# Performance work log

Measured on AMD Instinct MI355X. Metric: run time of the kernel, lower is better.

Reference implementation:

```python
import jax, jax.numpy as jnp
import numpy as np

JITTER = 1e-05
TOL = 1e-04
MAX_ITER = 10
TAYLOR_ORDER = 5


def _safe_eigh(A):
    # torch safe_eigh: first attempt always adds jitter*I (eigh on SPD never fails, so first try succeeds)
    D = A.shape[-1]
    return jnp.linalg.eigh(A + JITTER * jnp.eye(D, dtype=A.dtype))


def _rebuild(vecs, vals):
    # vecs @ diag(vals) @ vecs^T, batched
    return jnp.einsum('...ij,...j,...kj->...ik', vecs, vals, vecs)


def matrix_sqrt(A):
    vals, vecs = _safe_eigh(A)
    return _rebuild(vecs, jnp.sqrt(jnp.clip(vals, JITTER)))


def matrix_inv_sqrt(A):
    vals, vecs = _safe_eigh(A)
    return _rebuild(vecs, 1.0 / jnp.sqrt(jnp.clip(vals, JITTER)))


def enforce_spd(M):
    vals, vecs = _safe_eigh(M)
    M2 = _rebuild(vecs, jnp.clip(vals, JITTER))
    return (M2 + jnp.swapaxes(M2, -1, -2)) * 0.5


def expm_taylor(Xm):
    D = Xm.shape[-1]
    I = jnp.broadcast_to(jnp.eye(D, dtype=Xm.dtype), Xm.shape)
    out = I
    Xp = I
    fac = 1.0
    for i in range(1, TAYLOR_ORDER + 1):
        Xp = Xp @ Xm
        fac *= i
        out = out + Xp / fac
    return out


def karcher_mean(X):
    # X: (B, N, D, D) SPD matrices -> (B, D, D) Riemannian (Karcher) mean
    B, N, D, _ = X.shape
    G0 = X.mean(axis=1)

    def step(carry, _):
        G, done = carry
        G_sqrt = matrix_sqrt(G)
        G_is = matrix_inv_sqrt(G)
        # A[b,n] = G_is[b] @ X[b,n] @ G_is[b]
        A = jnp.einsum('bij,bnjk,bkl->bnil', G_is, X, G_is)
        vals, vecs = _safe_eigh(A)
        logA = _rebuild(vecs, jnp.log(jnp.clip(vals, JITTER)))  # (B,N,D,D)
        Delta = logA.mean(axis=1)  # (B,D,D)
        norm_Delta = jnp.sqrt(jnp.sum(Delta * Delta, axis=(-2, -1))).mean()
        G_new = enforce_spd(G_sqrt @ expm_taylor(Delta) @ G_sqrt)
        # torch updates G, THEN checks break -> freeze only once done was set in a previous iter
        G_next = jnp.where(done, G, G_new)
        done_next = jnp.logical_or(done, norm_Delta < TOL)
        return (G_next, done_next), None

    (G, _), _ = jax.lax.scan(step, (G0, jnp.array(False)), None, length=MAX_ITER)
    return G


def setup_inputs() -> dict:
    key = jax.random.key(0)
    B, N, D = 64, 512, 32
    A = jax.random.normal(key, (B, N, D, D), dtype=jnp.float32)
    # well-conditioned SPD inputs, as an SPD pooling layer would receive
    X = A @ jnp.swapaxes(A, -1, -2) / D + 0.5 * jnp.eye(D, dtype=jnp.float32)
    return {"X": X}


def reference(X) -> jnp.ndarray:
    return karcher_mean(X)
```

## Files before the change

kernel.cpp:

```cpp
#include <hip/hip_runtime.h>
#include <math.h>

#define BB 64
#define NN 512
#define DD 32
#define LD2 36
#define LDG 32
#define JIT 1e-5f
#define TOLF 1e-4f
#define MAXIT 10

__device__ __forceinline__ float bpf(int addr, float v) {
    return __int_as_float(__builtin_amdgcn_ds_bpermute(addr, __float_as_int(v)));
}

__device__ __forceinline__ void wsync() {
    __asm__ volatile("s_waitcnt lgkmcnt(0)" ::: "memory");
}

__device__ __forceinline__ void jac1(float a[16], int aself, int a32, int c,
                                     int maxsweep, float thr) {
#pragma unroll 1
    for (int sweep = 0; sweep < maxsweep; ++sweep) {
        float maxrel = 0.f;
#pragma unroll 1
        for (int m = 1; m < 32; ++m) {
            int am = aself ^ (m << 2);
            float pa[16];
#pragma unroll
            for (int i = 0; i < 16; ++i) pa[i] = bpf(am, a[i]);
            float gs = 0.f, gc = 0.f;
#pragma unroll
            for (int i = 0; i < 16; ++i) {
                gs = fmaf(a[i], a[i], gs);
                gc = fmaf(a[i], pa[i], gc);
            }
            gs += bpf(a32, gs);
            gc += bpf(a32, gc);
            float gp = bpf(am, gs);
            bool isP = c < (c ^ m);
            float gpp = isP ? gs : gp;
            float gqq = isP ? gp : gs;
            float rel = gc * gc * __builtin_amdgcn_rcpf(gpp * gqq);
            maxrel = fmaxf(maxrel, rel);
            float tau = (gqq - gpp) * (0.5f * __builtin_amdgcn_rcpf(gc));
            float den = fabsf(tau) + __builtin_amdgcn_sqrtf(fmaf(tau, tau, 1.f));
            float tt  = copysignf(__builtin_amdgcn_rcpf(den), tau);
            tt = (rel > 1e-24f) ? tt : 0.f;
            float cs  = __builtin_amdgcn_rsqf(fmaf(tt, tt, 1.f));
            float sn  = tt * cs;
            float sg = isP ? -sn : sn;
#pragma unroll
            for (int i = 0; i < 16; ++i) a[i] = fmaf(sg, pa[i], cs * a[i]);
        }
#pragma unroll
        for (int sh = 1; sh <= 32; sh <<= 1)
            maxrel = fmaxf(maxrel, bpf(aself ^ (sh << 2), maxrel));
        if (maxrel < thr) break;
    }
}

__device__ __forceinline__ void mm32w(const float* A, const float* B, float* C, int lane) {
    int r = lane >> 1, cb = (lane & 1) << 4;
    float acc[16];
#pragma unroll
    for (int j = 0; j < 16; ++j) acc[j] = 0.0f;
    for (int k = 0; k < DD; ++k) {
        float a = A[r * LD2 + k];
        const float4* Br = (const float4*)(B + k * LD2 + cb);
        float4 b0 = Br[0], b1 = Br[1], b2 = Br[2], b3 = Br[3];
        acc[0]  = fmaf(a, b0.x, acc[0]);  acc[1]  = fmaf(a, b0.y, acc[1]);
        acc[2]  = fmaf(a, b0.z, acc[2]);  acc[3]  = fmaf(a, b0.w, acc[3]);
        acc[4]  = fmaf(a, b1.x, acc[4]);  acc[5]  = fmaf(a, b1.y, acc[5]);
        acc[6]  = fmaf(a, b1.z, acc[6]);  acc[7]  = fmaf(a, b1.w, acc[7]);
        acc[8]  = fmaf(a, b2.x, acc[8]);  acc[9]  = fmaf(a, b2.y, acc[9]);
        acc[10] = fmaf(a, b2.z, acc[10]); acc[11] = fmaf(a, b2.w, acc[11]);
        acc[12] = fmaf(a, b3.x, acc[12]); acc[13] = fmaf(a, b3.y, acc[13]);
        acc[14] = fmaf(a, b3.z, acc[14]); acc[15] = fmaf(a, b3.w, acc[15]);
    }
    wsync();
    float4* Cr = (float4*)(C + r * LD2 + cb);
    Cr[0] = make_float4(acc[0],  acc[1],  acc[2],  acc[3]);
    Cr[1] = make_float4(acc[4],  acc[5],  acc[6],  acc[7]);
    Cr[2] = make_float4(acc[8],  acc[9],  acc[10], acc[11]);
    Cr[3] = make_float4(acc[12], acc[13], acc[14], acc[15]);
    wsync();
}


__global__ __launch_bounds__(256) void k0_zero(float* __restrict__ G, int* __restrict__ done,
                                               float* __restrict__ norm_acc, int* __restrict__ counter) {
    float4* Gb = (float4*)(G + blockIdx.x * 1024);
    Gb[threadIdx.x] = make_float4(0.f, 0.f, 0.f, 0.f);
    if (blockIdx.x == 0 && threadIdx.x == 0) { *done = 0; *norm_acc = 0.f; *counter = 0; }
}

__global__ __launch_bounds__(256) void k0_mean(const float* __restrict__ X, float* __restrict__ G) {
    int blk = blockIdx.x;
    int b = blk >> 3, chunk = blk & 7;
    int t = threadIdx.x;
    const float4* Xb = (const float4*)(X + ((size_t)(b * NN + chunk * 64)) * 1024);
    float4 acc = make_float4(0.f, 0.f, 0.f, 0.f);
    for (int n = 0; n < 64; ++n) {
        float4 v = Xb[n * 256 + t];
        acc.x += v.x; acc.y += v.y; acc.z += v.z; acc.w += v.w;
    }
    const float inv = 1.0f / NN;
    float* Gb = G + b * 1024 + t * 4;
    atomicAdd(Gb + 0, acc.x * inv);
    atomicAdd(Gb + 1, acc.y * inv);
    atomicAdd(Gb + 2, acc.z * inv);
    atomicAdd(Gb + 3, acc.w * inv);
}


__global__ __launch_bounds__(64) void k1_init(const float* __restrict__ G,
                                              float* __restrict__ Gs, float* __restrict__ Gis,
                                              float* __restrict__ Vg) {
    int b = blockIdx.x, lane = threadIdx.x;
    int c = lane & 31, h = lane >> 5;
    int aself = lane << 2, a32 = aself ^ 128;
    int r = lane >> 1, cb = (lane & 1) << 4;
    __shared__ __align__(16) float sW[DD * LD2];
    __shared__ float sc1[DD], sc2[DD];

    float a[16];
    {
        const float4* Gc = (const float4*)(G + b * 1024 + c * 32 + 16 * h);
        float4 v0 = Gc[0], v1 = Gc[1], v2 = Gc[2], v3 = Gc[3];
        a[0]=v0.x; a[1]=v0.y; a[2]=v0.z; a[3]=v0.w;
        a[4]=v1.x; a[5]=v1.y; a[6]=v1.z; a[7]=v1.w;
        a[8]=v2.x; a[9]=v2.y; a[10]=v2.z; a[11]=v2.w;
        a[12]=v3.x; a[13]=v3.y; a[14]=v3.z; a[15]=v3.w;
#pragma unroll
        for (int i = 0; i < 16; ++i)
            if (16 * h + i == c) a[i] += JIT;
    }
    jac1(a, aself, a32, c, 10, 1e-12f);
    float gs2 = 0.f;
#pragma unroll
    for (int i = 0; i < 16; ++i) gs2 = fmaf(a[i], a[i], gs2);
    gs2 += bpf(a32, gs2);
    float l  = __builtin_amdgcn_sqrtf(gs2);
    float lc = fmaxf(l, JIT);
    float ig = __builtin_amdgcn_rcpf(gs2);
    float c1 = __builtin_amdgcn_sqrtf(lc) * ig;
    float c2 = __builtin_amdgcn_rsqf(lc) * ig;
    if (Vg) {
        float inl = __builtin_amdgcn_rsqf(gs2);
        float4* Vp = (float4*)(Vg + b * 1024 + c * 32 + 16 * h);
        Vp[0] = make_float4(a[0]*inl,  a[1]*inl,  a[2]*inl,  a[3]*inl);
        Vp[1] = make_float4(a[4]*inl,  a[5]*inl,  a[6]*inl,  a[7]*inl);
        Vp[2] = make_float4(a[8]*inl,  a[9]*inl,  a[10]*inl, a[11]*inl);
        Vp[3] = make_float4(a[12]*inl, a[13]*inl, a[14]*inl, a[15]*inl);
    }
    {
        float4* wp = (float4*)&sW[c * LD2 + 16 * h];
        wp[0] = make_float4(a[0],  a[1],  a[2],  a[3]);
        wp[1] = make_float4(a[4],  a[5],  a[6],  a[7]);
        wp[2] = make_float4(a[8],  a[9],  a[10], a[11]);
        wp[3] = make_float4(a[12], a[13], a[14], a[15]);
        if (h == 0) { sc1[c] = c1; sc2[c] = c2; }
    }
    wsync();
    float a1[16], a2[16];
#pragma unroll
    for (int j = 0; j < 16; ++j) { a1[j] = 0.f; a2[j] = 0.f; }
    for (int k = 0; k < DD; ++k) {
        float wr = sW[k * LD2 + r];
        float t1 = wr * sc1[k], t2 = wr * sc2[k];
        const float4* Wc = (const float4*)&sW[k * LD2 + cb];
        float4 w0 = Wc[0], w1 = Wc[1], w2 = Wc[2], w3 = Wc[3];
        a1[0]+=t1*w0.x; a2[0]+=t2*w0.x;  a1[1]+=t1*w0.y; a2[1]+=t2*w0.y;
        a1[2]+=t1*w0.z; a2[2]+=t2*w0.z;  a1[3]+=t1*w0.w; a2[3]+=t2*w0.w;
        a1[4]+=t1*w1.x; a2[4]+=t2*w1.x;  a1[5]+=t1*w1.y; a2[5]+=t2*w1.y;
        a1[6]+=t1*w1.z; a2[6]+=t2*w1.z;  a1[7]+=t1*w1.w; a2[7]+=t2*w1.w;
        a1[8]+=t1*w2.x; a2[8]+=t2*w2.x;  a1[9]+=t1*w2.y; a2[9]+=t2*w2.y;
        a1[10]+=t1*w2.z; a2[10]+=t2*w2.z; a1[11]+=t1*w2.w; a2[11]+=t2*w2.w;
        a1[12]+=t1*w3.x; a2[12]+=t2*w3.x; a1[13]+=t1*w3.y; a2[13]+=t2*w3.y;
        a1[14]+=t1*w3.z; a2[14]+=t2*w3.z; a1[15]+=t1*w3.w; a2[15]+=t2*w3.w;
    }
    float4* Gsb  = (float4*)(Gs  + b * 1024 + lane * 16);
    float4* Gisb = (float4*)(Gis + b * 1024 + lane * 16);
#pragma unroll
    for (int j4 = 0; j4 < 4; ++j4) {
        Gsb[j4]  = make_float4(a1[4*j4], a1[4*j4+1], a1[4*j4+2], a1[4*j4+3]);
        Gisb[j4] = make_float4(a2[4*j4], a2[4*j4+1], a2[4*j4+2], a2[4*j4+3]);
    }
}


__global__ __launch_bounds__(512) void k2_log_acc(const float* __restrict__ X,
                                                  const float* __restrict__ Gis,
                                                  float* __restrict__ Part,
                                                  const int* __restrict__ done,
                                                  float* __restrict__ Vbuf,
                                                  int it) {
    if (*done) return;
    int b = blockIdx.x >> 4, grp = blockIdx.x & 15;
    int wv = threadIdx.x >> 6, lane = threadIdx.x & 63;
    int c = lane & 31, h = lane >> 5;
    int aself = lane << 2, a32 = aself ^ 128;

    __shared__ __align__(16) float sG[DD * LDG];
    __shared__ __align__(16) float sAall[8][DD * LD2];
    float* sA = sAall[wv];

    if (threadIdx.x < 256)
        ((float4*)sG)[threadIdx.x] = ((const float4*)(Gis + b * 1024))[threadIdx.x];
    __syncthreads();

    int r = lane >> 1, cb = (lane & 1) << 4;
    float dacc[16];
#pragma unroll
    for (int j = 0; j < 16; ++j) dacc[j] = 0.f;

#pragma unroll 1
    for (int nn = 0; nn < 4; ++nn) {
        int n = grp * 32 + wv * 4 + nn;
        {
            const float4* Xv = (const float4*)(X + ((size_t)(b * NN + n)) * 1024);
            float4 v0 = Xv[lane * 4 + 0], v1 = Xv[lane * 4 + 1];
            float4 v2 = Xv[lane * 4 + 2], v3 = Xv[lane * 4 + 3];
            wsync();
            int e = lane * 16;
            float* d0 = &sA[(e >> 5) * LD2 + (e & 31)];
            *((float4*)d0)        = v0;
            *((float4*)(d0 + 4))  = v1;
            *((float4*)(d0 + 8))  = v2;
            *((float4*)(d0 + 12)) = v3;
            wsync();
        }
        {
            float acc[16];
#pragma unroll
            for (int j = 0; j < 16; ++j) acc[j] = 0.f;
            for (int k = 0; k < DD; ++k) {
                float a = sG[k * LDG + r];
                const float4* Br = (const float4*)(sA + k * LD2 + cb);
                float4 b0 = Br[0], b1 = Br[1], b2 = Br[2], b3 = Br[3];
                acc[0]  = fmaf(a, b0.x, acc[0]);  acc[1]  = fmaf(a, b0.y, acc[1]);
                acc[2]  = fmaf(a, b0.z, acc[2]);  acc[3]  = fmaf(a, b0.w, acc[3]);
                acc[4]  = fmaf(a, b1.x, acc[4]);  acc[5]  = fmaf(a, b1.y, acc[5]);
                acc[6]  = fmaf(a, b1.z, acc[6]);  acc[7]  = fmaf(a, b1.w, acc[7]);
                acc[8]  = fmaf(a, b2.x, acc[8]);  acc[9]  = fmaf(a, b2.y, acc[9]);
                acc[10] = fmaf(a, b2.z, acc[10]); acc[11] = fmaf(a, b2.w, acc[11]);
                acc[12] = fmaf(a, b3.x, acc[12]); acc[13] = fmaf(a, b3.y, acc[13]);
                acc[14] = fmaf(a, b3.z, acc[14]); acc[15] = fmaf(a, b3.w, acc[15]);
            }
            wsync();
            float4* Cr = (float4*)(sA + r * LD2 + cb);
            Cr[0] = make_float4(acc[0],  acc[1],  acc[2],  acc[3]);
            Cr[1] = make_float4(acc[4],  acc[5],  acc[6],  acc[7]);
            Cr[2] = make_float4(acc[8],  acc[9],  acc[10], acc[11]);
            Cr[3] = make_float4(acc[12], acc[13], acc[14], acc[15]);
            wsync();
        }
        {
            float acc[16];
#pragma unroll
            for (int j = 0; j < 16; ++j) acc[j] = 0.f;
            for (int k = 0; k < DD; ++k) {
                float a = sA[r * LD2 + k];
                const float4* Br = (const float4*)(sG + k * LDG + cb);
                float4 b0 = Br[0], b1 = Br[1], b2 = Br[2], b3 = Br[3];
                acc[0]  = fmaf(a, b0.x, acc[0]);  acc[1]  = fmaf(a, b0.y, acc[1]);
                acc[2]  = fmaf(a, b0.z, acc[2]);  acc[3]  = fmaf(a, b0.w, acc[3]);
                acc[4]  = fmaf(a, b1.x, acc[4]);  acc[5]  = fmaf(a, b1.y, acc[5]);
                acc[6]  = fmaf(a, b1.z, acc[6]);  acc[7]  = fmaf(a, b1.w, acc[7]);
                acc[8]  = fmaf(a, b2.x, acc[8]);  acc[9]  = fmaf(a, b2.y, acc[9]);
                acc[10] = fmaf(a, b2.z, acc[10]); acc[11] = fmaf(a, b2.w, acc[11]);
                acc[12] = fmaf(a, b3.x, acc[12]); acc[13] = fmaf(a, b3.y, acc[13]);
                acc[14] = fmaf(a, b3.z, acc[14]); acc[15] = fmaf(a, b3.w, acc[15]);
            }
            wsync();
            float4* Cr = (float4*)(sA + r * LD2 + cb);
            Cr[0] = make_float4(acc[0],  acc[1],  acc[2],  acc[3]);
            Cr[1] = make_float4(acc[4],  acc[5],  acc[6],  acc[7]);
            Cr[2] = make_float4(acc[8],  acc[9],  acc[10], acc[11]);
            Cr[3] = make_float4(acc[12], acc[13], acc[14], acc[15]);
            wsync();
        }
        float a[16];
        if (it == 0) {
            const float4* cp = (const float4*)&sA[c * LD2 + 16 * h];
            float4 t0 = cp[0], t1 = cp[1], t2 = cp[2], t3 = cp[3];
            float tr[16] = { t0.x,t0.y,t0.z,t0.w, t1.x,t1.y,t1.z,t1.w,
                             t2.x,t2.y,t2.z,t2.w, t3.x,t3.y,t3.z,t3.w };
#pragma unroll
            for (int i = 0; i < 16; ++i) {
                int row = 16 * h + i;
                float v = 0.5f * (sA[row * LD2 + c] + tr[i]);
                if (row == c) v = tr[i] + JIT;
                a[i] = v;
            }
        } else {
            float v[32];
            {
                const float4* Vp = (const float4*)(Vbuf + ((size_t)(b * NN + n)) * 1024 + c * 32);
#pragma unroll
                for (int j4 = 0; j4 < 8; ++j4) {
                    float4 t = Vp[j4];
                    v[4*j4] = t.x; v[4*j4+1] = t.y; v[4*j4+2] = t.z; v[4*j4+3] = t.w;
                }
            }
#pragma unroll
            for (int i = 0; i < 16; ++i) {
                const float4* Ar = (const float4*)&sA[(16 * h + i) * LD2];
                float s = 0.f;
#pragma unroll
                for (int j4 = 0; j4 < 8; ++j4) {
                    float4 q = Ar[j4];
                    s = fmaf(q.x, v[4*j4],   s);
                    s = fmaf(q.y, v[4*j4+1], s);
                    s = fmaf(q.z, v[4*j4+2], s);
                    s = fmaf(q.w, v[4*j4+3], s);
                }
                a[i] = fmaf(JIT, v[16 * h + i], s);
            }
        }

        jac1(a, aself, a32, c, 8, (it == 0) ? 3e-10f : 1e-8f);

        {
            float gs2 = 0.f;
#pragma unroll
            for (int i = 0; i < 16; ++i) gs2 = fmaf(a[i], a[i], gs2);
            gs2 += bpf(a32, gs2);
            float gs2c = fmaxf(gs2, JIT * JIT);
            float tk = 0.5f * logf(gs2c) * __builtin_amdgcn_rcpf(gs2);
            if (Vbuf) {
                float inl = __builtin_amdgcn_rsqf(gs2);
                float4* Vp = (float4*)(Vbuf + ((size_t)(b * NN + n)) * 1024 + c * 32 + 16 * h);
                Vp[0] = make_float4(a[0]*inl,  a[1]*inl,  a[2]*inl,  a[3]*inl);
                Vp[1] = make_float4(a[4]*inl,  a[5]*inl,  a[6]*inl,  a[7]*inl);
                Vp[2] = make_float4(a[8]*inl,  a[9]*inl,  a[10]*inl, a[11]*inl);
                Vp[3] = make_float4(a[12]*inl, a[13]*inl, a[14]*inl, a[15]*inl);
            }
            wsync();
            float4* wp = (float4*)&sA[c * LD2 + 16 * h];
            wp[0] = make_float4(a[0],  a[1],  a[2],  a[3]);
            wp[1] = make_float4(a[4],  a[5],  a[6],  a[7]);
            wp[2] = make_float4(a[8],  a[9],  a[10], a[11]);
            wp[3] = make_float4(a[12], a[13], a[14], a[15]);
            if (h == 0) sA[c * LD2 + 32] = tk;
            wsync();
            for (int k = 0; k < DD; ++k) {
                float t1 = sA[k * LD2 + r] * sA[k * LD2 + 32];
                const float4* Wr = (const float4*)&sA[k * LD2 + cb];
                float4 w0 = Wr[0], w1 = Wr[1], w2 = Wr[2], w3 = Wr[3];
                dacc[0]  = fmaf(t1, w0.x, dacc[0]);  dacc[1]  = fmaf(t1, w0.y, dacc[1]);
                dacc[2]  = fmaf(t1, w0.z, dacc[2]);  dacc[3]  = fmaf(t1, w0.w, dacc[3]);
                dacc[4]  = fmaf(t1, w1.x, dacc[4]);  dacc[5]  = fmaf(t1, w1.y, dacc[5]);
                dacc[6]  = fmaf(t1, w1.z, dacc[6]);  dacc[7]  = fmaf(t1, w1.w, dacc[7]);
                dacc[8]  = fmaf(t1, w2.x, dacc[8]);  dacc[9]  = fmaf(t1, w2.y, dacc[9]);
                dacc[10] = fmaf(t1, w2.z, dacc[10]); dacc[11] = fmaf(t1, w2.w, dacc[11]);
                dacc[12] = fmaf(t1, w3.x, dacc[12]); dacc[13] = fmaf(t1, w3.y, dacc[13]);
                dacc[14] = fmaf(t1, w3.z, dacc[14]); dacc[15] = fmaf(t1, w3.w, dacc[15]);
            }
        }
    }
    wsync();

    {
        float4* fp = (float4*)&sA[lane * 16];
        fp[0] = make_float4(dacc[0],  dacc[1],  dacc[2],  dacc[3]);
        fp[1] = make_float4(dacc[4],  dacc[5],  dacc[6],  dacc[7]);
        fp[2] = make_float4(dacc[8],  dacc[9],  dacc[10], dacc[11]);
        fp[3] = make_float4(dacc[12], dacc[13], dacc[14], dacc[15]);
    }
    __syncthreads();
    if (threadIdx.x < 256) {
        int t = threadIdx.x;
        float4 s0 = ((float4*)sAall[0])[t];
        float4 s1 = ((float4*)sAall[1])[t];
        float4 s2 = ((float4*)sAall[2])[t];
        float4 s3 = ((float4*)sAall[3])[t];
        float4 s4 = ((float4*)sAall[4])[t];
        float4 s5 = ((float4*)sAall[5])[t];
        float4 s6 = ((float4*)sAall[6])[t];
        float4 s7 = ((float4*)sAall[7])[t];
        float4 s;
        s.x = ((s0.x + s1.x) + (s2.x + s3.x)) + ((s4.x + s5.x) + (s6.x + s7.x));
        s.y = ((s0.y + s1.y) + (s2.y + s3.y)) + ((s4.y + s5.y) + (s6.y + s7.y));
        s.z = ((s0.z + s1.z) + (s2.z + s3.z)) + ((s4.z + s5.z) + (s6.z + s7.z));
        s.w = ((s0.w + s1.w) + (s2.w + s3.w)) + ((s4.w + s5.w) + (s6.w + s7.w));
        ((float4*)(Part + (size_t)blockIdx.x * 1024))[t] = s;
    }
}


__global__ __launch_bounds__(64) void k31_update(float* __restrict__ G,
                                                 float* __restrict__ Gs,
                                                 float* __restrict__ Gis,
                                                 const float* __restrict__ Part,
                                                 float* __restrict__ norm_acc,
                                                 int* __restrict__ counter,
                                                 int* __restrict__ done,
                                                 float* __restrict__ Vg) {
    if (*done) return;
    int b = blockIdx.x, lane = threadIdx.x;
    int c = lane & 31, h = lane >> 5;
    int aself = lane << 2, a32 = aself ^ 128;
    int r = lane >> 1, cb = (lane & 1) << 4;
    __shared__ __align__(16) float s0[DD * LD2], s1[DD * LD2], s2[DD * LD2];
    __shared__ float scg[DD], scs[DD], sci[DD];

    float d[16];
#pragma unroll
    for (int j = 0; j < 16; ++j) d[j] = 0.f;
#pragma unroll 1
    for (int g = 0; g < 16; ++g) {
        const float4* P = (const float4*)(Part + (size_t)(b * 16 + g) * 1024 + lane * 16);
        float4 p0 = P[0], p1 = P[1], p2 = P[2], p3 = P[3];
        d[0]+=p0.x; d[1]+=p0.y; d[2]+=p0.z; d[3]+=p0.w;
        d[4]+=p1.x; d[5]+=p1.y; d[6]+=p1.z; d[7]+=p1.w;
        d[8]+=p2.x; d[9]+=p2.y; d[10]+=p2.z; d[11]+=p2.w;
        d[12]+=p3.x; d[13]+=p3.y; d[14]+=p3.z; d[15]+=p3.w;
    }
    const float inv = 1.0f / NN;
    float sumsq = 0.f;
#pragma unroll
    for (int j = 0; j < 16; ++j) { d[j] *= inv; sumsq = fmaf(d[j], d[j], sumsq); }
#pragma unroll
    for (int sh = 1; sh <= 32; sh <<= 1) sumsq += bpf(aself ^ (sh << 2), sumsq);
    if (lane == 0) atomicAdd(norm_acc, sqrtf(sumsq));

    {
        float4* dp = (float4*)&s0[r * LD2 + cb];
        dp[0] = make_float4(d[0],  d[1],  d[2],  d[3]);
        dp[1] = make_float4(d[4],  d[5],  d[6],  d[7]);
        dp[2] = make_float4(d[8],  d[9],  d[10], d[11]);
        dp[3] = make_float4(d[12], d[13], d[14], d[15]);
    }
    wsync();

    float outr[16];
#pragma unroll
    for (int j = 0; j < 16; ++j)
        outr[j] = ((cb + j) == r ? 1.0f : 0.0f) + d[j];
    float fac = 1.0f;
#pragma unroll 1
    for (int i = 2; i <= 5; ++i) {
        fac *= (float)i;
        float acc[16];
#pragma unroll
        for (int j = 0; j < 16; ++j) acc[j] = 0.f;
        const float* Xp = (i == 2) ? s0 : s1;
        for (int k = 0; k < DD; ++k) {
            float av = Xp[r * LD2 + k];
            const float4* Br = (const float4*)&s0[k * LD2 + cb];
            float4 b0 = Br[0], b1 = Br[1], b2 = Br[2], b3 = Br[3];
            acc[0]+=av*b0.x; acc[1]+=av*b0.y; acc[2]+=av*b0.z; acc[3]+=av*b0.w;
            acc[4]+=av*b1.x; acc[5]+=av*b1.y; acc[6]+=av*b1.z; acc[7]+=av*b1.w;
            acc[8]+=av*b2.x; acc[9]+=av*b2.y; acc[10]+=av*b2.z; acc[11]+=av*b2.w;
            acc[12]+=av*b3.x; acc[13]+=av*b3.y; acc[14]+=av*b3.z; acc[15]+=av*b3.w;
        }
        float invf = 1.0f / fac;
#pragma unroll
        for (int j = 0; j < 16; ++j) outr[j] = fmaf(acc[j], invf, outr[j]);
        wsync();
        float4* dp = (float4*)&s1[r * LD2 + cb];
        dp[0] = make_float4(acc[0],  acc[1],  acc[2],  acc[3]);
        dp[1] = make_float4(acc[4],  acc[5],  acc[6],  acc[7]);
        dp[2] = make_float4(acc[8],  acc[9],  acc[10], acc[11]);
        dp[3] = make_float4(acc[12], acc[13], acc[14], acc[15]);
        wsync();
    }
    {
        float4* dp = (float4*)&s0[r * LD2 + cb];
        dp[0] = make_float4(outr[0],  outr[1],  outr[2],  outr[3]);
        dp[1] = make_float4(outr[4],  outr[5],  outr[6],  outr[7]);
        dp[2] = make_float4(outr[8],  outr[9],  outr[10], outr[11]);
        dp[3] = make_float4(outr[12], outr[13], outr[14], outr[15]);
        const float4* Gsb = (const float4*)(Gs + b * 1024);
#pragma unroll
        for (int j4 = 0; j4 < 4; ++j4) {
            float4 v = Gsb[lane * 4 + j4];
            int e = lane * 16 + j4 * 4;
            *((float4*)&s1[(e >> 5) * LD2 + (e & 31)]) = v;
        }
    }
    wsync();
    mm32w(s1, s0, s2, lane);
    mm32w(s2, s1, s0, lane);

    float a[16];
    if (Vg == nullptr) {
#pragma unroll
        for (int i = 0; i < 16; ++i) {
            int row = 16 * h + i;
            float own = s0[c * LD2 + row];
            float v = 0.5f * (s0[row * LD2 + c] + own);
            if (row == c) v = own + JIT;
            a[i] = v;
        }
    } else {
        float v[32];
        {
            const float4* Vp = (const float4*)(Vg + b * 1024 + c * 32);
#pragma unroll
            for (int j4 = 0; j4 < 8; ++j4) {
                float4 t = Vp[j4];
                v[4*j4] = t.x; v[4*j4+1] = t.y; v[4*j4+2] = t.z; v[4*j4+3] = t.w;
            }
        }
#pragma unroll
        for (int i = 0; i < 16; ++i) {
            const float4* Mr = (const float4*)&s0[(16 * h + i) * LD2];
            float s = 0.f;
#pragma unroll
            for (int j4 = 0; j4 < 8; ++j4) {
                float4 q = Mr[j4];
                s = fmaf(q.x, v[4*j4],   s);
                s = fmaf(q.y, v[4*j4+1], s);
                s = fmaf(q.z, v[4*j4+2], s);
                s = fmaf(q.w, v[4*j4+3], s);
            }
            a[i] = fmaf(JIT, v[16 * h + i], s);
        }
    }
    jac1(a, aself, a32, c, 10, 1e-12f);
    float gs2 = 0.f;
#pragma unroll
    for (int i = 0; i < 16; ++i) gs2 = fmaf(a[i], a[i], gs2);
    gs2 += bpf(a32, gs2);
    float l = __builtin_amdgcn_sqrtf(gs2);
    float clipl = fmaxf(l, JIT);
    float ig = __builtin_amdgcn_rcpf(gs2);
    float tg = clipl * ig;
    float sh = clipl + JIT;
    float ts = __builtin_amdgcn_sqrtf(sh) * ig;
    float ti = __builtin_amdgcn_rsqf(sh) * ig;
    if (Vg) {
        float inl = __builtin_amdgcn_rsqf(gs2);
        float4* Vp = (float4*)(Vg + b * 1024 + c * 32 + 16 * h);
        Vp[0] = make_float4(a[0]*inl,  a[1]*inl,  a[2]*inl,  a[3]*inl);
        Vp[1] = make_float4(a[4]*inl,  a[5]*inl,  a[6]*inl,  a[7]*inl);
        Vp[2] = make_float4(a[8]*inl,  a[9]*inl,  a[10]*inl, a[11]*inl);
        Vp[3] = make_float4(a[12]*inl, a[13]*inl, a[14]*inl, a[15]*inl);
    }
    wsync();
    {
        float4* wp = (float4*)&s1[c * LD2 + 16 * h];
        wp[0] = make_float4(a[0],  a[1],  a[2],  a[3]);
        wp[1] = make_float4(a[4],  a[5],  a[6],  a[7]);
        wp[2] = make_float4(a[8],  a[9],  a[10], a[11]);
        wp[3] = make_float4(a[12], a[13], a[14], a[15]);
        if (h == 0) { scg[c] = tg; scs[c] = ts; sci[c] = ti; }
    }
    wsync();
    float gg[16], gsv[16], giv[16];
#pragma unroll
    for (int j = 0; j < 16; ++j) { gg[j] = 0.f; gsv[j] = 0.f; giv[j] = 0.f; }
    for (int k = 0; k < DD; ++k) {
        float wr = s1[k * LD2 + r];
        float cg = wr * scg[k], cs2 = wr * scs[k], ci = wr * sci[k];
        const float4* Wc = (const float4*)&s1[k * LD2 + cb];
        float4 w0 = Wc[0], w1 = Wc[1], w2 = Wc[2], w3 = Wc[3];
        gg[0]+=cg*w0.x; gsv[0]+=cs2*w0.x; giv[0]+=ci*w0.x;
        gg[1]+=cg*w0.y; gsv[1]+=cs2*w0.y; giv[1]+=ci*w0.y;
        gg[2]+=cg*w0.z; gsv[2]+=cs2*w0.z; giv[2]+=ci*w0.z;
        gg[3]+=cg*w0.w; gsv[3]+=cs2*w0.w; giv[3]+=ci*w0.w;
        gg[4]+=cg*w1.x; gsv[4]+=cs2*w1.x; giv[4]+=ci*w1.x;
        gg[5]+=cg*w1.y; gsv[5]+=cs2*w1.y; giv[5]+=ci*w1.y;
        gg[6]+=cg*w1.z; gsv[6]+=cs2*w1.z; giv[6]+=ci*w1.z;
        gg[7]+=cg*w1.w; gsv[7]+=cs2*w1.w; giv[7]+=ci*w1.w;
        gg[8]+=cg*w2.x; gsv[8]+=cs2*w2.x; giv[8]+=ci*w2.x;
        gg[9]+=cg*w2.y; gsv[9]+=cs2*w2.y; giv[9]+=ci*w2.y;
        gg[10]+=cg*w2.z; gsv[10]+=cs2*w2.z; giv[10]+=ci*w2.z;
        gg[11]+=cg*w2.w; gsv[11]+=cs2*w2.w; giv[11]+=ci*w2.w;
        gg[12]+=cg*w3.x; gsv[12]+=cs2*w3.x; giv[12]+=ci*w3.x;
        gg[13]+=cg*w3.y; gsv[13]+=cs2*w3.y; giv[13]+=ci*w3.y;
        gg[14]+=cg*w3.z; gsv[14]+=cs2*w3.z; giv[14]+=ci*w3.z;
        gg[15]+=cg*w3.w; gsv[15]+=cs2*w3.w; giv[15]+=ci*w3.w;
    }
    float4* Gb   = (float4*)(G   + b * 1024 + lane * 16);
    float4* Gsb  = (float4*)(Gs  + b * 1024 + lane * 16);
    float4* Gib  = (float4*)(Gis + b * 1024 + lane * 16);
#pragma unroll
    for (int j4 = 0; j4 < 4; ++j4) {
        Gb[j4]  = make_float4(gg[4*j4],  gg[4*j4+1],  gg[4*j4+2],  gg[4*j4+3]);
        Gsb[j4] = make_float4(gsv[4*j4], gsv[4*j4+1], gsv[4*j4+2], gsv[4*j4+3]);
        Gib[j4] = make_float4(giv[4*j4], giv[4*j4+1], giv[4*j4+2], giv[4*j4+3]);
    }

    __threadfence();
    if (lane == 0) {
        int ret = atomicAdd(counter, 1);
        if (ret == BB - 1) {
            float nm = atomicAdd(norm_acc, 0.f);
            if (nm * (1.0f / BB) < TOLF) *done = 1;
            *norm_acc = 0.f;
            *counter = 0;
            __threadfence();
        }
    }
}

__global__ __launch_bounds__(256) void k5_out(const float* __restrict__ G, float* __restrict__ out) {
    int i = blockIdx.x * 256 + threadIdx.x;
    out[i] = G[i];
}

extern "C" void kernel_launch(void* const* d_in, const int* in_sizes, int n_in,
                              void* d_out, int out_size, void* d_ws, size_t ws_size,
                              hipStream_t stream) {
    const float* X = (const float*)d_in[0];
    float* ws = (float*)d_ws;
    float* G     = ws;
    float* Gs    = ws + 65536;
    float* Gis   = ws + 2 * 65536;
    float* Part  = ws + 3 * 65536;
    float* norm_acc = ws + 3 * 65536 + 1048576;
    int*   counter  = (int*)(norm_acc + 1);
    int*   done     = (int*)(norm_acc + 2);
    size_t base_floats = (size_t)3 * 65536 + 1048576 + 16;
    float* Vg   = (ws_size >= (base_floats + (size_t)BB * 1024) * sizeof(float))
                  ? (ws + base_floats) : nullptr;
    float* Vbuf = (ws_size >= (base_floats + (size_t)BB * 1024 + (size_t)BB * NN * 1024) * sizeof(float))
                  ? (ws + base_floats + (size_t)BB * 1024) : nullptr;

    k0_zero<<<64, 256, 0, stream>>>(G, done, norm_acc, counter);
    k0_mean<<<512, 256, 0, stream>>>(X, G);
    k1_init<<<64, 64, 0, stream>>>(G, Gs, Gis, Vg);
    for (int it = 0; it < MAXIT; ++it) {
        int it_eff = (Vbuf != nullptr) ? it : 0;
        k2_log_acc<<<1024, 512, 0, stream>>>(X, Gis, Part, done, Vbuf, it_eff);
        k31_update<<<64, 64, 0, stream>>>(G, Gs, Gis, Part, norm_acc, counter, done, Vg);
    }
    k5_out<<<256, 256, 0, stream>>>(G, (float*)d_out);
}
```

Measured before the change: 4.902 ms.

## Fuse per-batch update into log-accumulate kernel via last-block-done counter

Removes the separate k31_update launch by having the last of the 16 blocks per batch (tracked with a per-batch atomic counter) perform the Taylor expm, the Jacobi eigendecomposition and the G/Gs/Gis rebuild inside k2_log_acc. The three fused accumulations are split into three sequential passes to cut register pressure, and launch bounds now request 6 blocks per CU. The first-iteration tighter Jacobi threshold is also dropped, using 1e-8 for every iteration. This saves one launch per iteration but serializes the update tail on a single wave, and the looser first-sweep threshold may affect accuracy.

After: 4.869 ms. Within noise of the previous version (-0.7%).

```diff
diff --git a/kernel.cpp b/kernel.cpp
--- a/kernel.cpp
+++ b/kernel.cpp
@@ -89,10 +89,14 @@
 
 
 __global__ __launch_bounds__(256) void k0_zero(float* __restrict__ G, int* __restrict__ done,
-                                               float* __restrict__ norm_acc, int* __restrict__ counter) {
+                                               float* __restrict__ norm_acc, int* __restrict__ cnt_all,
+                                               int* __restrict__ cnt_b) {
     float4* Gb = (float4*)(G + blockIdx.x * 1024);
     Gb[threadIdx.x] = make_float4(0.f, 0.f, 0.f, 0.f);
-    if (blockIdx.x == 0 && threadIdx.x == 0) { *done = 0; *norm_acc = 0.f; *counter = 0; }
+    if (blockIdx.x == 0) {
+        if (threadIdx.x == 0) { *done = 0; *norm_acc = 0.f; *cnt_all = 0; }
+        if (threadIdx.x < BB) cnt_b[threadIdx.x] = 0;
+    }
 }
 
 __global__ __launch_bounds__(256) void k0_mean(const float* __restrict__ X, float* __restrict__ G) {
@@ -190,12 +194,16 @@
 }
 
 
-__global__ __launch_bounds__(512) void k2_log_acc(const float* __restrict__ X,
-                                                  const float* __restrict__ Gis,
-                                                  float* __restrict__ Part,
-                                                  const int* __restrict__ done,
-                                                  float* __restrict__ Vbuf,
-                                                  int it) {
+__global__ __launch_bounds__(512, 6) void k2_log_acc(const float* __restrict__ X,
+                                                     float* G, float* Gs, float* Gis,
+                                                     float* __restrict__ Part,
+                                                     int* __restrict__ done,
+                                                     float* __restrict__ Vbuf,
+                                                     float* __restrict__ Vg,
+                                                     float* __restrict__ norm_acc,
+                                                     int* __restrict__ cnt_all,
+                                                     int* __restrict__ cnt_b,
+                                                     int it) {
     if (*done) return;
     int b = blockIdx.x >> 4, grp = blockIdx.x & 15;
     int wv = threadIdx.x >> 6, lane = threadIdx.x & 63;
@@ -320,7 +328,7 @@
             }
         }
 
-        jac1(a, aself, a32, c, 8, (it == 0) ? 3e-10f : 1e-8f);
+        jac1(a, aself, a32, c, 8, 1e-8f);
 
         {
             float gs2 = 0.f;
@@ -387,213 +395,202 @@
         s.w = ((s0.w + s1.w) + (s2.w + s3.w)) + ((s4.w + s5.w) + (s6.w + s7.w));
         ((float4*)(Part + (size_t)blockIdx.x * 1024))[t] = s;
     }
-}
-
-
-__global__ __launch_bounds__(64) void k31_update(float* __restrict__ G,
-                                                 float* __restrict__ Gs,
-                                                 float* __restrict__ Gis,
-                                                 const float* __restrict__ Part,
-                                                 float* __restrict__ norm_acc,
-                                                 int* __restrict__ counter,
-                                                 int* __restrict__ done,
-                                                 float* __restrict__ Vg) {
-    if (*done) return;
-    int b = blockIdx.x, lane = threadIdx.x;
-    int c = lane & 31, h = lane >> 5;
-    int aself = lane << 2, a32 = aself ^ 128;
-    int r = lane >> 1, cb = (lane & 1) << 4;
-    __shared__ __align__(16) float s0[DD * LD2], s1[DD * LD2], s2[DD * LD2];
-    __shared__ float scg[DD], scs[DD], sci[DD];
-
-    float d[16];
-#pragma unroll
-    for (int j = 0; j < 16; ++j) d[j] = 0.f;
+
+    int* winp = (int*)sG;
+    if (threadIdx.x == 0) *winp = 0;
+    __syncthreads();
+    if (threadIdx.x == 0) {
+        __threadfence();
+        int ret = atomicAdd(&cnt_b[b], 1);
+        if (ret == 15) { *winp = 1; cnt_b[b] = 0; }
+    }
+    __syncthreads();
+    if (*winp == 0) return;
+    if (threadIdx.x >= 64) return;
+    __threadfence();
+
+    {
+        float* s0 = sAall[0];
+        float* s1 = sAall[1];
+        float* s2 = sAall[2];
+        float* scof = sAall[3];
+
+        float d[16];
+#pragma unroll
+        for (int j = 0; j < 16; ++j) d[j] = 0.f;
 #pragma unroll 1
-    for (int g = 0; g < 16; ++g) {
-        const float4* P = (const float4*)(Part + (size_t)(b * 16 + g) * 1024 + lane * 16);
-        float4 p0 = P[0], p1 = P[1], p2 = P[2], p3 = P[3];
-        d[0]+=p0.x; d[1]+=p0.y; d[2]+=p0.z; d[3]+=p0.w;
-        d[4]+=p1.x; d[5]+=p1.y; d[6]+=p1.z; d[7]+=p1.w;
-        d[8]+=p2.x; d[9]+=p2.y; d[10]+=p2.z; d[11]+=p2.w;
-        d[12]+=p3.x; d[13]+=p3.y; d[14]+=p3.z; d[15]+=p3.w;
-    }
-    const float inv = 1.0f / NN;
-    float sumsq = 0.f;
-#pragma unroll
-    for (int j = 0; j < 16; ++j) { d[j] *= inv; sumsq = fmaf(d[j], d[j], sumsq); }
-#pragma unroll
-    for (int sh = 1; sh <= 32; sh <<= 1) sumsq += bpf(aself ^ (sh << 2), sumsq);
-    if (lane == 0) atomicAdd(norm_acc, sqrtf(sumsq));
-
-    {
-        float4* dp = (float4*)&s0[r * LD2 + cb];
-        dp[0] = make_float4(d[0],  d[1],  d[2],  d[3]);
-        dp[1] = make_float4(d[4],  d[5],  d[6],  d[7]);
-        dp[2] = make_float4(d[8],  d[9],  d[10], d[11]);
-        dp[3] = make_float4(d[12], d[13], d[14], d[15]);
-    }
-    wsync();
-
-    float outr[16];
-#pragma unroll
-    for (int j = 0; j < 16; ++j)
-        outr[j] = ((cb + j) == r ? 1.0f : 0.0f) + d[j];
-    float fac = 1.0f;
+        for (int g = 0; g < 16; ++g) {
+            const float4* P = (const float4*)(Part + (size_t)(b * 16 + g) * 1024 + lane * 16);
+            float4 p0 = P[0], p1 = P[1], p2 = P[2], p3 = P[3];
+            d[0]+=p0.x; d[1]+=p0.y; d[2]+=p0.z; d[3]+=p0.w;
+            d[4]+=p1.x; d[5]+=p1.y; d[6]+=p1.z; d[7]+=p1.w;
+            d[8]+=p2.x; d[9]+=p2.y; d[10]+=p2.z; d[11]+=p2.w;
+            d[12]+=p3.x; d[13]+=p3.y; d[14]+=p3.z; d[15]+=p3.w;
+        }
+        const float inv = 1.0f / NN;
+        float sumsq = 0.f;
+#pragma unroll
+        for (int j = 0; j < 16; ++j) { d[j] *= inv; sumsq = fmaf(d[j], d[j], sumsq); }
+#pragma unroll
+        for (int sh = 1; sh <= 32; sh <<= 1) sumsq += bpf(aself ^ (sh << 2), sumsq);
+        if (lane == 0) atomicAdd(norm_acc, sqrtf(sumsq));
+
+        wsync();
+        {
+            float4* dp = (float4*)&s0[r * LD2 + cb];
+            dp[0] = make_float4(d[0],  d[1],  d[2],  d[3]);
+            dp[1] = make_float4(d[4],  d[5],  d[6],  d[7]);
+            dp[2] = make_float4(d[8],  d[9],  d[10], d[11]);
+            dp[3] = make_float4(d[12], d[13], d[14], d[15]);
+        }
+        wsync();
+
+        float outr[16];
+#pragma unroll
+        for (int j = 0; j < 16; ++j)
+            outr[j] = ((cb + j) == r ? 1.0f : 0.0f) + d[j];
+        float fac = 1.0f;
 #pragma unroll 1
-    for (int i = 2; i <= 5; ++i) {
-        fac *= (float)i;
-        float acc[16];
-#pragma unroll
-        for (int j = 0; j < 16; ++j) acc[j] = 0.f;
-        const float* Xp = (i == 2) ? s0 : s1;
-        for (int k = 0; k < DD; ++k) {
-            float av = Xp[r * LD2 + k];
-            const float4* Br = (const float4*)&s0[k * LD2 + cb];
-            float4 b0 = Br[0], b1 = Br[1], b2 = Br[2], b3 = Br[3];
-            acc[0]+=av*b0.x; acc[1]+=av*b0.y; acc[2]+=av*b0.z; acc[3]+=av*b0.w;
-            acc[4]+=av*b1.x; acc[5]+=av*b1.y; acc[6]+=av*b1.z; acc[7]+=av*b1.w;
-            acc[8]+=av*b2.x; acc[9]+=av*b2.y; acc[10]+=av*b2.z; acc[11]+=av*b2.w;
-            acc[12]+=av*b3.x; acc[13]+=av*b3.y; acc[14]+=av*b3.z; acc[15]+=av*b3.w;
-        }
-        float invf = 1.0f / fac;
-#pragma unroll
-        for (int j = 0; j < 16; ++j) outr[j] = fmaf(acc[j], invf, outr[j]);
+        for (int i = 2; i <= 5; ++i) {
+            fac *= (float)i;
+            float acc[16];
+#pragma unroll
+            for (int j = 0; j < 16; ++j) acc[j] = 0.f;
+            const float* Xp = (i == 2) ? s0 : s1;
+            for (int k = 0; k < DD; ++k) {
+                float av = Xp[r * LD2 + k];
+                const float4* Br = (const float4*)&s0[k * LD2 + cb];
+                float4 b0 = Br[0], b1 = Br[1], b2 = Br[2], b3 = Br[3];
+                acc[0]+=av*b0.x; acc[1]+=av*b0.y; acc[2]+=av*b0.z; acc[3]+=av*b0.w;
+                acc[4]+=av*b1.x; acc[5]+=av*b1.y; acc[6]+=av*b1.z; acc[7]+=av*b1.w;
+                acc[8]+=av*b2.x; acc[9]+=av*b2.y; acc[10]+=av*b2.z; acc[11]+=av*b2.w;
+                acc[12]+=av*b3.x; acc[13]+=av*b3.y; acc[14]+=av*b3.z; acc[15]+=av*b3.w;
+            }
+            float invf = 1.0f / fac;
+#pragma unroll
+            for (int j = 0; j < 16; ++j) outr[j] = fmaf(acc[j], invf, outr[j]);
+            wsync();
+            float4* dp = (float4*)&s1[r * LD2 + cb];
+            dp[0] = make_float4(acc[0],  acc[1],  acc[2],  acc[3]);
+            dp[1] = make_float4(acc[4],  acc[5],  acc[6],  acc[7]);
+            dp[2] = make_float4(acc[8],  acc[9],  acc[10], acc[11]);
+            dp[3] = make_float4(acc[12], acc[13], acc[14], acc[15]);
+            wsync();
+        }
+        {
+            float4* dp = (float4*)&s0[r * LD2 + cb];
+            dp[0] = make_float4(outr[0],  outr[1],  outr[2],  outr[3]);
+            dp[1] = make_float4(outr[4],  outr[5],  outr[6],  outr[7]);
+            dp[2] = make_float4(outr[8],  outr[9],  outr[10], outr[11]);
+            dp[3] = make_float4(outr[12], outr[13], outr[14], outr[15]);
+            const float4* Gsb = (const float4*)(Gs + b * 1024);
+#pragma unroll
+            for (int j4 = 0; j4 < 4; ++j4) {
+                float4 v = Gsb[lane * 4 + j4];
+                int e = lane * 16 + j4 * 4;
+                *((float4*)&s1[(e >> 5) * LD2 + (e & 31)]) = v;
+            }
+        }
         wsync();
-        float4* dp = (float4*)&s1[r * LD2 + cb];
-        dp[0] = make_float4(acc[0],  acc[1],  acc[2],  acc[3]);
-        dp[1] = make_float4(acc[4],  acc[5],  acc[6],  acc[7]);
-        dp[2] = make_float4(acc[8],  acc[9],  acc[10], acc[11]);
-        dp[3] = make_float4(acc[12], acc[13], acc[14], acc[15]);
+        mm32w(s1, s0, s2, lane);
+        mm32w(s2, s1, s0, lane);
+
+        float a[16];
+        if (Vg == nullptr) {
+#pragma unroll
+            for (int i = 0; i < 16; ++i) {
+                int row = 16 * h + i;
+                float own = s0[c * LD2 + row];
+                float v = 0.5f * (s0[row * LD2 + c] + own);
+                if (row == c) v = own + JIT;
+                a[i] = v;
+            }
+        } else {
+            float v[32];
+            {
+                const float4* Vp = (const float4*)(Vg + b * 1024 + c * 32);
+#pragma unroll
+                for (int j4 = 0; j4 < 8; ++j4) {
+                    float4 t = Vp[j4];
+                    v[4*j4] = t.x; v[4*j4+1] = t.y; v[4*j4+2] = t.z; v[4*j4+3] = t.w;
+                }
+            }
+#pragma unroll
+            for (int i = 0; i < 16; ++i) {
+                const float4* Mr = (const float4*)&s0[(16 * h + i) * LD2];
+                float s = 0.f;
+#pragma unroll
+                for (int j4 = 0; j4 < 8; ++j4) {
+                    float4 q = Mr[j4];
+                    s = fmaf(q.x, v[4*j4],   s);
+                    s = fmaf(q.y, v[4*j4+1], s);
+                    s = fmaf(q.z, v[4*j4+2], s);
+                    s = fmaf(q.w, v[4*j4+3], s);
+                }
+                a[i] = fmaf(JIT, v[16 * h + i], s);
+            }
+        }
+        jac1(a, aself, a32, c, 10, 1e-12f);
+        float gs2 = 0.f;
+#pragma unroll
+        for (int i = 0; i < 16; ++i) gs2 = fmaf(a[i], a[i], gs2);
+        gs2 += bpf(a32, gs2);
+        float l = __builtin_amdgcn_sqrtf(gs2);
+        float clipl = fmaxf(l, JIT);
+        float ig = __builtin_amdgcn_rcpf(gs2);
+        float tg = clipl * ig;
+        float sh = clipl + JIT;
+        float ts = __builtin_amdgcn_sqrtf(sh) * ig;
+        float ti = __builtin_amdgcn_rsqf(sh) * ig;
+        if (Vg) {
+            float inl = __builtin_amdgcn_rsqf(gs2);
+            float4* Vp = (float4*)(Vg + b * 1024 + c * 32 + 16 * h);
+            Vp[0] = make_float4(a[0]*inl,  a[1]*inl,  a[2]*inl,  a[3]*inl);
+            Vp[1] = make_float4(a[4]*inl,  a[5]*inl,  a[6]*inl,  a[7]*inl);
+            Vp[2] = make_float4(a[8]*inl,  a[9]*inl,  a[10]*inl, a[11]*inl);
+            Vp[3] = make_float4(a[12]*inl, a[13]*inl, a[14]*inl, a[15]*inl);
+        }
         wsync();
-    }
-    {
-        float4* dp = (float4*)&s0[r * LD2 + cb];
-        dp[0] = make_float4(outr[0],  outr[1],  outr[2],  outr[3]);
-        dp[1] = make_float4(outr[4],  outr[5],  outr[6],  outr[7]);
-        dp[2] = make_float4(outr[8],  outr[9],  outr[10], outr[11]);
-        dp[3] = make_float4(outr[12], outr[13], outr[14], outr[15]);
-        const float4* Gsb = (const float4*)(Gs + b * 1024);
-#pragma unroll
-        for (int j4 = 0; j4 < 4; ++j4) {
-            float4 v = Gsb[lane * 4 + j4];
-            int e = lane * 16 + j4 * 4;
-            *((float4*)&s1[(e >> 5) * LD2 + (e & 31)]) = v;
-        }
-    }
-    wsync();
-    mm32w(s1, s0, s2, lane);
-    mm32w(s2, s1, s0, lane);
-
-    float a[16];
-    if (Vg == nullptr) {
-#pragma unroll
-        for (int i = 0; i < 16; ++i) {
-            int row = 16 * h + i;
-            float own = s0[c * LD2 + row];
-            float v = 0.5f * (s0[row * LD2 + c] + own);
-            if (row == c) v = own + JIT;
-            a[i] = v;
-        }
-    } else {
-        float v[32];
         {
-            const float4* Vp = (const float4*)(Vg + b * 1024 + c * 32);
-#pragma unroll
-            for (int j4 = 0; j4 < 8; ++j4) {
-                float4 t = Vp[j4];
-                v[4*j4] = t.x; v[4*j4+1] = t.y; v[4*j4+2] = t.z; v[4*j4+3] = t.w;
-            }
-        }
-#pragma unroll
-        for (int i = 0; i < 16; ++i) {
-            const float4* Mr = (const float4*)&s0[(16 * h + i) * LD2];
-            float s = 0.f;
-#pragma unroll
-            for (int j4 = 0; j4 < 8; ++j4) {
-                float4 q = Mr[j4];
-                s = fmaf(q.x, v[4*j4],   s);
-                s = fmaf(q.y, v[4*j4+1], s);
-                s = fmaf(q.z, v[4*j4+2], s);
-                s = fmaf(q.w, v[4*j4+3], s);
-            }
-            a[i] = fmaf(JIT, v[16 * h + i], s);
-        }
-    }
-    jac1(a, aself, a32, c, 10, 1e-12f);
-    float gs2 = 0.f;
-#pragma unroll
-    for (int i = 0; i < 16; ++i) gs2 = fmaf(a[i], a[i], gs2);
-    gs2 += bpf(a32, gs2);
-    float l = __builtin_amdgcn_sqrtf(gs2);
-    float clipl = fmaxf(l, JIT);
-    float ig = __builtin_amdgcn_rcpf(gs2);
-    float tg = clipl * ig;
-    float sh = clipl + JIT;
-    float ts = __builtin_amdgcn_sqrtf(sh) * ig;
-    float ti = __builtin_amdgcn_rsqf(sh) * ig;
-    if (Vg) {
-        float inl = __builtin_amdgcn_rsqf(gs2);
-        float4* Vp = (float4*)(Vg + b * 1024 + c * 32 + 16 * h);
-        Vp[0] = make_float4(a[0]*inl,  a[1]*inl,  a[2]*inl,  a[3]*inl);
-        Vp[1] = make_float4(a[4]*inl,  a[5]*inl,  a[6]*inl,  a[7]*inl);
-        Vp[2] = make_float4(a[8]*inl,  a[9]*inl,  a[10]*inl, a[11]*inl);
-        Vp[3] = make_float4(a[12]*inl, a[13]*inl, a[14]*inl, a[15]*inl);
-    }
-    wsync();
-    {
-        float4* wp = (float4*)&s1[c * LD2 + 16 * h];
-        wp[0] = make_float4(a[0],  a[1],  a[2],  a[3]);
-        wp[1] = make_float4(a[4],  a[5],  a[6],  a[7]);
-        wp[2] = make_float4(a[8],  a[9],  a[10], a[11]);
-        wp[3] = make_float4(a[12], a[13], a[14], a[15]);
-        if (h == 0) { scg[c] = tg; scs[c] = ts; sci[c] = ti; }
-    }
-    wsync();
-    float gg[16], gsv[16], giv[16];
-#pragma unroll
-    for (int j = 0; j < 16; ++j) { gg[j] = 0.f; gsv[j] = 0.f; giv[j] = 0.f; }
-    for (int k = 0; k < DD; ++k) {
-        float wr = s1[k * LD2 + r];
-        float cg = wr * scg[k], cs2 = wr * scs[k], ci = wr * sci[k];
-        const float4* Wc = (const float4*)&s1[k * LD2 + cb];
-        float4 w0 = Wc[0], w1 = Wc[1], w2 = Wc[2], w3 = Wc[3];
-        gg[0]+=cg*w0.x; gsv[0]+=cs2*w0.x; giv[0]+=ci*w0.x;
-        gg[1]+=cg*w0.y; gsv[1]+=cs2*w0.y; giv[1]+=ci*w0.y;
-        gg[2]+=cg*w0.z; gsv[2]+=cs2*w0.z; giv[2]+=ci*w0.z;
-        gg[3]+=cg*w0.w; gsv[3]+=cs2*w0.w; giv[3]+=ci*w0.w;
-        gg[4]+=cg*w1.x; gsv[4]+=cs2*w1.x; giv[4]+=ci*w1.x;
-        gg[5]+=cg*w1.y; gsv[5]+=cs2*w1.y; giv[5]+=ci*w1.y;
-        gg[6]+=cg*w1.z; gsv[6]+=cs2*w1.z; giv[6]+=ci*w1.z;
-        gg[7]+=cg*w1.w; gsv[7]+=cs2*w1.w; giv[7]+=ci*w1.w;
-        gg[8]+=cg*w2.x; gsv[8]+=cs2*w2.x; giv[8]+=ci*w2.x;
-        gg[9]+=cg*w2.y; gsv[9]+=cs2*w2.y; giv[9]+=ci*w2.y;
-        gg[10]+=cg*w2.z; gsv[10]+=cs2*w2.z; giv[10]+=ci*w2.z;
-        gg[11]+=cg*w2.w; gsv[11]+=cs2*w2.w; giv[11]+=ci*w2.w;
-        gg[12]+=cg*w3.x; gsv[12]+=cs2*w3.x; giv[12]+=ci*w3.x;
-        gg[13]+=cg*w3.y; gsv[13]+=cs2*w3.y; giv[13]+=ci*w3.y;
-        gg[14]+=cg*w3.z; gsv[14]+=cs2*w3.z; giv[14]+=ci*w3.z;
-        gg[15]+=cg*w3.w; gsv[15]+=cs2*w3.w; giv[15]+=ci*w3.w;
-    }
-    float4* Gb   = (float4*)(G   + b * 1024 + lane * 16);
-    float4* Gsb  = (float4*)(Gs  + b * 1024 + lane * 16);
-    float4* Gib  = (float4*)(Gis + b * 1024 + lane * 16);
-#pragma unroll
-    for (int j4 = 0; j4 < 4; ++j4) {
-        Gb[j4]  = make_float4(gg[4*j4],  gg[4*j4+1],  gg[4*j4+2],  gg[4*j4+3]);
-        Gsb[j4] = make_float4(gsv[4*j4], gsv[4*j4+1], gsv[4*j4+2], gsv[4*j4+3]);
-        Gib[j4] = make_float4(giv[4*j4], giv[4*j4+1], giv[4*j4+2], giv[4*j4+3]);
-    }
-
-    __threadfence();
-    if (lane == 0) {
-        int ret = atomicAdd(counter, 1);
-        if (ret == BB - 1) {
-            float nm = atomicAdd(norm_acc, 0.f);
-            if (nm * (1.0f / BB) < TOLF) *done = 1;
-            *norm_acc = 0.f;
-            *counter = 0;
-            __threadfence();
+            float4* wp = (float4*)&s1[c * LD2 + 16 * h];
+            wp[0] = make_float4(a[0],  a[1],  a[2],  a[3]);
+            wp[1] = make_float4(a[4],  a[5],  a[6],  a[7]);
+            wp[2] = make_float4(a[8],  a[9],  a[10], a[11]);
+            wp[3] = make_float4(a[12], a[13], a[14], a[15]);
+            if (h == 0) { scof[c] = tg; scof[32 + c] = ts; scof[64 + c] = ti; }
+        }
+        wsync();
+#pragma unroll 1
+        for (int pass = 0; pass < 3; ++pass) {
+            float g[16];
+#pragma unroll
+            for (int j = 0; j < 16; ++j) g[j] = 0.f;
+            for (int k = 0; k < DD; ++k) {
+                float t1 = s1[k * LD2 + r] * scof[pass * 32 + k];
+                const float4* Wc = (const float4*)&s1[k * LD2 + cb];
+                float4 w0 = Wc[0], w1 = Wc[1], w2 = Wc[2], w3 = Wc[3];
+                g[0]+=t1*w0.x; g[1]+=t1*w0.y; g[2]+=t1*w0.z; g[3]+=t1*w0.w;
+                g[4]+=t1*w1.x; g[5]+=t1*w1.y; g[6]+=t1*w1.z; g[7]+=t1*w1.w;
+                g[8]+=t1*w2.x; g[9]+=t1*w2.y; g[10]+=t1*w2.z; g[11]+=t1*w2.w;
+                g[12]+=t1*w3.x; g[13]+=t1*w3.y; g[14]+=t1*w3.z; g[15]+=t1*w3.w;
+            }
+            float* dst = (pass == 0) ? G : (pass == 1) ? Gs : Gis;
+            float4* Db = (float4*)(dst + b * 1024 + lane * 16);
+#pragma unroll
+            for (int j4 = 0; j4 < 4; ++j4)
+                Db[j4] = make_float4(g[4*j4], g[4*j4+1], g[4*j4+2], g[4*j4+3]);
+        }
+
+        __threadfence();
+        if (lane == 0) {
+            int r2 = atomicAdd(cnt_all, 1);
+            if (r2 == BB - 1) {
+                float nm = atomicAdd(norm_acc, 0.f);
+                if (nm * (1.0f / BB) < TOLF) *done = 1;
+                *norm_acc = 0.f;
+                *cnt_all = 0;
+                __threadfence();
+            }
         }
     }
 }
@@ -613,21 +610,22 @@
     float* Gis   = ws + 2 * 65536;
     float* Part  = ws + 3 * 65536;
     float* norm_acc = ws + 3 * 65536 + 1048576;
-    int*   counter  = (int*)(norm_acc + 1);
+    int*   cnt_all  = (int*)(norm_acc + 1);
     int*   done     = (int*)(norm_acc + 2);
-    size_t base_floats = (size_t)3 * 65536 + 1048576 + 16;
+    int*   cnt_b    = (int*)(norm_acc + 3);
+    size_t base_floats = (size_t)3 * 65536 + 1048576 + 80;
     float* Vg   = (ws_size >= (base_floats + (size_t)BB * 1024) * sizeof(float))
                   ? (ws + base_floats) : nullptr;
     float* Vbuf = (ws_size >= (base_floats + (size_t)BB * 1024 + (size_t)BB * NN * 1024) * sizeof(float))
                   ? (ws + base_floats + (size_t)BB * 1024) : nullptr;
 
-    k0_zero<<<64, 256, 0, stream>>>(G, done, norm_acc, counter);
+    k0_zero<<<64, 256, 0, stream>>>(G, done, norm_acc, cnt_all, cnt_b);
     k0_mean<<<512, 256, 0, stream>>>(X, G);
     k1_init<<<64, 64, 0, stream>>>(G, Gs, Gis, Vg);
     for (int it = 0; it < MAXIT; ++it) {
         int it_eff = (Vbuf != nullptr) ? it : 0;
-        k2_log_acc<<<1024, 512, 0, stream>>>(X, Gis, Part, done, Vbuf, it_eff);
-        k31_update<<<64, 64, 0, stream>>>(G, Gs, Gis, Part, norm_acc, counter, done, Vg);
+        k2_log_acc<<<1024, 512, 0, stream>>>(X, G, Gs, Gis, Part, done, Vbuf, Vg,
+                                             norm_acc, cnt_all, cnt_b, it_eff);
     }
     k5_out<<<256, 256, 0, stream>>>(G, (float*)d_out);
 }
```
